# Kernel tuning notes

Measured on AMD Instinct MI355X. Metric: run time of the kernel, lower is better.

The kernel has to match this reference:

```python
import jax, jax.numpy as jnp
import numpy as np

T = 2048          # tokens (prefill, single sequence)
H = 4096          # hidden_size
NH = 32           # num attention heads
NKV = 8           # num kv heads (GQA)
HD = H // NH      # head_dim = 128
EPS = 1e-5
THETA = 10000.0


def setup_inputs() -> dict:
    key = jax.random.key(0)
    k0, k1, k2 = jax.random.split(key, 3)
    return {
        "positions": jnp.arange(T, dtype=jnp.int64 if jax.config.jax_enable_x64 else jnp.int32),
        "hidden_states": jax.random.normal(k0, (T, H), dtype=jnp.float32),
        "w_qkv": jax.random.normal(k1, (H, (NH + 2 * NKV) * HD), dtype=jnp.float32) * 0.02,
        "w_o": jax.random.normal(k2, (NH * HD, H), dtype=jnp.float32) * 0.02,
        "q_norm_w": jnp.ones((NH, HD), dtype=jnp.float32),
        "k_norm_w": jnp.ones((NKV, HD), dtype=jnp.float32),
    }


def _layer_norm(x, w, eps):
    # x: [T, n_heads, HD], w: [n_heads, HD]; mean/var over last dim, fp32 math
    xf = x.astype(jnp.float32)
    mean = xf.mean(-1, keepdims=True)
    var = jnp.square(xf - mean).mean(-1, keepdims=True)
    y = (xf - mean) * jax.lax.rsqrt(var + eps)
    return (w.astype(jnp.float32)[None] * y).astype(x.dtype)


def _rope_interleaved(x, positions):
    # non-neox (GPT-J) style: rotate interleaved pairs. x: [T, n, HD]
    inv_freq = 1.0 / (THETA ** (jnp.arange(0, HD, 2, dtype=jnp.float32) / HD))  # [HD/2]
    freqs = positions.astype(jnp.float32)[:, None] * inv_freq[None, :]          # [T, HD/2]
    cos = jnp.cos(freqs)[:, None, :]  # [T,1,HD/2]
    sin = jnp.sin(freqs)[:, None, :]
    x1 = x[..., 0::2]
    x2 = x[..., 1::2]
    o1 = x1 * cos - x2 * sin
    o2 = x2 * cos + x1 * sin
    return jnp.stack([o1, o2], axis=-1).reshape(x.shape)


def reference(positions, hidden_states, w_qkv, w_o, q_norm_w, k_norm_w):
    qkv = hidden_states @ w_qkv  # [T, (NH+2*NKV)*HD]
    q, k, v = jnp.split(qkv, [NH * HD, (NH + NKV) * HD], axis=-1)
    q = q.reshape(T, NH, HD)
    k = k.reshape(T, NKV, HD)
    v = v.reshape(T, NKV, HD)

    # per-head qk LayerNorm
    q = _layer_norm(q, q_norm_w, EPS)
    k = _layer_norm(k, k_norm_w, EPS)

    # non-neox RoPE
    q = _rope_interleaved(q, positions)
    k = _rope_interleaved(k, positions)

    # GQA: expand kv heads to NH
    rep = NH // NKV
    k = jnp.repeat(k, rep, axis=1)  # [T, NH, HD]
    v = jnp.repeat(v, rep, axis=1)

    scale = HD ** -0.5
    scores = jnp.einsum("qhd,khd->hqk", q * scale, k)  # [NH, T, T]
    causal = jnp.tril(jnp.ones((T, T), dtype=bool))
    scores = jnp.where(causal[None], scores, jnp.finfo(scores.dtype).min)
    probs = jax.nn.softmax(scores, axis=-1)
    attn = jnp.einsum("hqk,khd->qhd", probs, v).reshape(T, NH * HD)

    return attn @ w_o  # [T, H]
```

## Files before the change

### kernel.cpp

```cpp
#include <hip/hip_runtime.h>
#include <cstdint>
#include <cstddef>

#define T_SEQ   2048
#define H_DIM   4096
#define NH_Q    32
#define NKV_H   8
#define HD_     128
#define QKV_N   6144
#define EPS_F   1e-5f
#define ATT_SCALE 0.08838834764831845f
#define LN_THETA  9.210340371976184f

typedef __attribute__((ext_vector_type(8))) short bf16x8;
typedef __attribute__((ext_vector_type(4))) float f32x4;

static __device__ __forceinline__ unsigned short f2bf(float f) {
  union { float f; uint32_t u; } v; v.f = f;
  uint32_t u = v.u;
  u += 0x7fff + ((u >> 16) & 1);
  return (unsigned short)(u >> 16);
}
static __device__ __forceinline__ float bf2f(unsigned short h) {
  union { uint32_t u; float f; } v; v.u = ((uint32_t)h) << 16;
  return v.f;
}

static __device__ __forceinline__ void gld_lds16(const void* g, void* l) {
  __builtin_amdgcn_global_load_lds(
      (const __attribute__((address_space(1))) unsigned int*)g,
      (__attribute__((address_space(3))) unsigned int*)l, 16, 0, 0);
}

__global__ void convert_bf16_kernel(const float* __restrict__ in,
                                    unsigned short* __restrict__ out, int n4) {
  int i = blockIdx.x * blockDim.x + threadIdx.x;
  if (i < n4) {
    float4 f = *(const float4*)(in + (size_t)i * 4);
    ushort4 o;
    o.x = f2bf(f.x); o.y = f2bf(f.y); o.z = f2bf(f.z); o.w = f2bf(f.w);
    *(ushort4*)(out + (size_t)i * 4) = o;
  }
}

__global__ void transpose_bf16_kernel(const float* __restrict__ in,
                                      unsigned short* __restrict__ out,
                                      int R, int C) {
  __shared__ float tile[32][33];
  int c0 = blockIdx.x * 32, r0 = blockIdx.y * 32;
  int tx = threadIdx.x, ty = threadIdx.y;
  for (int i = 0; i < 32; i += 8)
    tile[ty + i][tx] = in[(size_t)(r0 + ty + i) * C + c0 + tx];
  __syncthreads();
  for (int i = 0; i < 32; i += 8)
    out[(size_t)(c0 + ty + i) * R + r0 + tx] = f2bf(tile[tx][ty + i]);
}

template <int FC, int PHASES, bool BF16OUT>
__global__ __launch_bounds__(512) void gemm256_kernel(
    const unsigned short* __restrict__ A, const unsigned short* __restrict__ Bt,
    void* __restrict__ Cp, int M, int N, int K) {
  constexpr int BN = FC * 64;
  constexpr int FR_PER = 8 / PHASES;
  __shared__ unsigned short As[2][256 * 64];
  __shared__ unsigned short Bs[2][BN * 64];
  const int tid = threadIdx.x, lane = tid & 63, wid = tid >> 6;
  const int wm = wid >> 2, wn = wid & 3;
  const int g = lane >> 4, s = lane & 15, s7 = s & 7;
  const int m0 = blockIdx.y * 256, n0 = blockIdx.x * BN;
  const int NT = K >> 6;

  const int lr = lane >> 3, lc = lane & 7;
  const size_t srcoff = (size_t)lr * K + (size_t)((lc ^ lr) * 8);

  auto stage_A_half = [&](const unsigned short* gbase, unsigned short* dst,
                          int h) {
    const int r0 = wid * 32 + h * 16;
    gld_lds16(gbase + (size_t)r0 * K + srcoff, dst + r0 * 64);
    gld_lds16(gbase + (size_t)(r0 + 8) * K + srcoff, dst + (r0 + 8) * 64);
  };
  auto stage_B = [&](const unsigned short* gbase, unsigned short* dst) {
#pragma unroll
    for (int j = 0; j < FC; j++) {
      const int r0 = wid * (FC * 8) + j * 8;
      gld_lds16(gbase + (size_t)r0 * K + srcoff, dst + r0 * 64);
    }
  };

  const int aroff = (wm * 128 + s) * 64;
  const int broff = (wn * FC * 16 + s) * 64;
  const int ck0 = ((0 * 4 + g) ^ s7) * 8;
  const int ck1 = ((1 * 4 + g) ^ s7) * 8;

  f32x4 acc[8][FC] = {};

  stage_A_half(A + (size_t)m0 * K, &As[0][0], 0);
  stage_A_half(A + (size_t)m0 * K, &As[0][0], 1);
  stage_B(Bt + (size_t)n0 * K, &Bs[0][0]);
  stage_B(Bt + (size_t)n0 * K + 64, &Bs[1][0]);
  if constexpr (FC == 2) asm volatile("s_waitcnt vmcnt(2)" ::: "memory");
  else                   asm volatile("s_waitcnt vmcnt(3)" ::: "memory");
  __builtin_amdgcn_s_barrier();

  auto tile_step = [&](int t, unsigned short* cA, unsigned short* cB,
                       unsigned short* nA) {
    const int k0 = t << 6;
    bf16x8 bfr[FC][2];
#pragma unroll
    for (int p = 0; p < PHASES; p++) {
      if (p == 0) {
#pragma unroll
        for (int fc = 0; fc < FC; fc++) {
          bfr[fc][0] = *(const bf16x8*)(cB + broff + fc * 1024 + ck0);
          bfr[fc][1] = *(const bf16x8*)(cB + broff + fc * 1024 + ck1);
        }
      }
      bf16x8 a[FR_PER][2];
#pragma unroll
      for (int i = 0; i < FR_PER; i++) {
        const int fr = p * FR_PER + i;
        a[i][0] = *(const bf16x8*)(cA + aroff + fr * 1024 + ck0);
        a[i][1] = *(const bf16x8*)(cA + aroff + fr * 1024 + ck1);
      }
      if (t + 1 < NT) {
        if (PHASES == 2) {
          if (p == 0) {
            stage_A_half(A + (size_t)m0 * K + k0 + 64, nA, 0);
            stage_A_half(A + (size_t)m0 * K + k0 + 64, nA, 1);
          }
        } else {
          if (p == 0) stage_A_half(A + (size_t)m0 * K + k0 + 64, nA, 0);
          if (p == 1) stage_A_half(A + (size_t)m0 * K + k0 + 64, nA, 1);
        }
      }
      if (p == PHASES - 1 && t + 2 < NT)
        stage_B(Bt + (size_t)n0 * K + k0 + 128, cB);
      __builtin_amdgcn_s_barrier();
      __builtin_amdgcn_s_setprio(1);
#pragma unroll
      for (int i = 0; i < FR_PER; i++) {
        const int fr = p * FR_PER + i;
#pragma unroll
        for (int fc = 0; fc < FC; fc++)
          acc[fr][fc] = __builtin_amdgcn_mfma_f32_16x16x32_bf16(
              a[i][0], bfr[fc][0], acc[fr][fc], 0, 0, 0);
      }
#pragma unroll
      for (int i = 0; i < FR_PER; i++) {
        const int fr = p * FR_PER + i;
#pragma unroll
        for (int fc = 0; fc < FC; fc++)
          acc[fr][fc] = __builtin_amdgcn_mfma_f32_16x16x32_bf16(
              a[i][1], bfr[fc][1], acc[fr][fc], 0, 0, 0);
      }
      __builtin_amdgcn_s_setprio(0);
      if (p == PHASES - 1) {
        if (t + 2 < NT) {
          if constexpr (FC == 2) asm volatile("s_waitcnt vmcnt(2)" ::: "memory");
          else                   asm volatile("s_waitcnt vmcnt(3)" ::: "memory");
        } else {
          asm volatile("s_waitcnt vmcnt(0)" ::: "memory");
        }
      }
      __builtin_amdgcn_s_barrier();
    }
  };

  for (int t = 0; t < NT; t += 2) {
    tile_step(t,     &As[0][0], &Bs[0][0], &As[1][0]);
    tile_step(t + 1, &As[1][0], &Bs[1][0], &As[0][0]);
  }

#pragma unroll
  for (int fr = 0; fr < 8; fr++)
#pragma unroll
    for (int fc = 0; fc < FC; fc++)
#pragma unroll
      for (int r = 0; r < 4; r++) {
        int m = m0 + wm * 128 + fr * 16 + g * 4 + r;
        int n = n0 + wn * FC * 16 + fc * 16 + s;
        float v = acc[fr][fc][r];
        if (BF16OUT) ((unsigned short*)Cp)[(size_t)m * N + n] = f2bf(v);
        else         ((float*)Cp)[(size_t)m * N + n] = v;
      }
}

__global__ __launch_bounds__(256) void ln_rope_kernel(
    unsigned short* __restrict__ qkv, const int* __restrict__ positions,
    const float* __restrict__ qw, const float* __restrict__ kw) {
  const int wid = threadIdx.x >> 6, lane = threadIdx.x & 63;
  const int rid = blockIdx.x * 4 + wid;
  const int t = rid / 40, hh = rid % 40;
  const bool isq = hh < NH_Q;
  const int col = isq ? hh * HD_ : H_DIM + (hh - NH_Q) * HD_;
  unsigned short* row = qkv + (size_t)t * QKV_N + col;

  uint32_t both = *(const uint32_t*)(row + lane * 2);
  float x1 = bf2f((unsigned short)(both & 0xffff));
  float x2 = bf2f((unsigned short)(both >> 16));
  float ssum = x1 + x2, ssq = x1 * x1 + x2 * x2;
  for (int off = 1; off < 64; off <<= 1) {
    ssum += __shfl_xor(ssum, off, 64);
    ssq  += __shfl_xor(ssq,  off, 64);
  }
  float mean = ssum * (1.0f / HD_);
  float var  = ssq * (1.0f / HD_) - mean * mean;
  float rs = rsqrtf(var + EPS_F);
  const float* w = isq ? (qw + hh * HD_) : (kw + (hh - NH_Q) * HD_);
  float2 wv = *(const float2*)(w + lane * 2);
  float y1 = (x1 - mean) * rs * wv.x;
  float y2 = (x2 - mean) * rs * wv.y;
  float pos = (float)positions[t];
  float inv = __expf(-((float)(2 * lane) * (1.0f / HD_)) * LN_THETA);
  float fr = pos * inv;
  float c = cosf(fr), sn = sinf(fr);
  float o1 = y1 * c - y2 * sn;
  float o2 = y2 * c + y1 * sn;
  if (isq) { o1 *= ATT_SCALE; o2 *= ATT_SCALE; }
  *(uint32_t*)(row + lane * 2) =
      (uint32_t)f2bf(o1) | ((uint32_t)f2bf(o2) << 16);
}

__global__ void vt_kernel(const unsigned short* __restrict__ qkv,
                          unsigned short* __restrict__ vt) {
  __shared__ unsigned short tile[32][33];
  const int kvh = blockIdx.z;
  const int t0 = blockIdx.x * 32, d0 = blockIdx.y * 32;
  const int tx = threadIdx.x, ty = threadIdx.y;
  for (int i = 0; i < 32; i += 8)
    tile[ty + i][tx] =
        qkv[(size_t)(t0 + ty + i) * QKV_N + H_DIM + NKV_H * HD_ + kvh * HD_ + d0 + tx];
  __syncthreads();
  for (int i = 0; i < 32; i += 8)
    vt[((size_t)kvh * HD_ + d0 + ty + i) * T_SEQ + t0 + tx] = tile[tx][ty + i];
}

__global__ __launch_bounds__(256) void attn_kernel(
    const unsigned short* __restrict__ qkv, const unsigned short* __restrict__ vt,
    unsigned short* __restrict__ out) {
  __shared__ unsigned short Ks[64 * 136];
  __shared__ unsigned short Vs[128 * 72];
  __shared__ unsigned short Ps[4][16 * 72];
  const int tid = threadIdx.x, lane = tid & 63, wid = tid >> 6;
  const int g = lane >> 4, s = lane & 15;
  const int h = blockIdx.y;
  const int kvh = h >> 2;
  const int NQT = T_SEQ / 64;

  for (int half = 0; half < 2; half++) {
    const int qt = (half == 0) ? (int)blockIdx.x : NQT - 1 - (int)blockIdx.x;
    const int q0 = qt * 64;

    bf16x8 qf[4];
    {
      const unsigned short* qrow =
          qkv + (size_t)(q0 + wid * 16 + s) * QKV_N + h * HD_;
      for (int ks = 0; ks < 4; ks++)
        qf[ks] = *(const bf16x8*)(qrow + ks * 32 + g * 8);
    }
    f32x4 o[8] = {};
    float m_i[4], l_i[4];
    for (int r = 0; r < 4; r++) { m_i[r] = -1e30f; l_i[r] = 0.f; }

    const int ktiles = qt + 1;
    for (int kt = 0; kt < ktiles; kt++) {
      const int k0 = kt * 64;
      __syncthreads();
      {
        int kr = tid >> 4, kc = tid & 15;
        for (int p = 0; p < 4; p++) {
          bf16x8 v = *(const bf16x8*)(qkv + (size_t)(k0 + kr + p * 16) * QKV_N +
                                      H_DIM + kvh * HD_ + kc * 8);
          *(bf16x8*)&Ks[(kr + p * 16) * 136 + kc * 8] = v;
        }
        int vr = tid >> 3, vc = tid & 7;
        for (int p = 0; p < 4; p++) {
          bf16x8 v = *(const bf16x8*)(vt + ((size_t)kvh * HD_ + vr + p * 32) * T_SEQ +
                                      k0 + vc * 8);
          *(bf16x8*)&Vs[(vr + p * 32) * 72 + vc * 8] = v;
        }
      }
      __syncthreads();
      f32x4 sa[4] = {};
      __builtin_amdgcn_s_setprio(1);
      for (int nt = 0; nt < 4; nt++)
        for (int ks = 0; ks < 4; ks++) {
          bf16x8 kb = *(const bf16x8*)&Ks[(nt * 16 + s) * 136 + ks * 32 + g * 8];
          sa[nt] = __builtin_amdgcn_mfma_f32_16x16x32_bf16(qf[ks], kb, sa[nt], 0, 0, 0);
        }
      __builtin_amdgcn_s_setprio(0);
      if (kt == ktiles - 1) {
        for (int nt = 0; nt < 4; nt++)
          for (int r = 0; r < 4; r++)
            if (k0 + nt * 16 + s > q0 + wid * 16 + g * 4 + r) sa[nt][r] = -1e30f;
      }
      float alpha[4];
      for (int r = 0; r < 4; r++) {
        float mx = fmaxf(fmaxf(sa[0][r], sa[1][r]), fmaxf(sa[2][r], sa[3][r]));
        for (int off = 1; off < 16; off <<= 1) mx = fmaxf(mx, __shfl_xor(mx, off, 64));
        float mn = fmaxf(m_i[r], mx);
        alpha[r] = __expf(m_i[r] - mn);
        m_i[r] = mn;
        float rsum = 0.f;
        for (int nt = 0; nt < 4; nt++) {
          float p = __expf(sa[nt][r] - mn);
          sa[nt][r] = p;
          rsum += p;
        }
        for (int off = 1; off < 16; off <<= 1) rsum += __shfl_xor(rsum, off, 64);
        l_i[r] = l_i[r] * alpha[r] + rsum;
      }
      for (int nt = 0; nt < 4; nt++)
        for (int r = 0; r < 4; r++)
          Ps[wid][(g * 4 + r) * 72 + nt * 16 + s] = f2bf(sa[nt][r]);
      for (int ot = 0; ot < 8; ot++)
        for (int r = 0; r < 4; r++) o[ot][r] *= alpha[r];
      __syncthreads();
      __builtin_amdgcn_s_setprio(1);
      for (int ot = 0; ot < 8; ot++)
        for (int ks = 0; ks < 2; ks++) {
          bf16x8 pa = *(const bf16x8*)&Ps[wid][s * 72 + ks * 32 + g * 8];
          bf16x8 vb = *(const bf16x8*)&Vs[(ot * 16 + s) * 72 + ks * 32 + g * 8];
          o[ot] = __builtin_amdgcn_mfma_f32_16x16x32_bf16(pa, vb, o[ot], 0, 0, 0);
        }
      __builtin_amdgcn_s_setprio(0);
    }
    const size_t obase = (size_t)(q0 + wid * 16);
    for (int ot = 0; ot < 8; ot++)
      for (int r = 0; r < 4; r++) {
        float v = o[ot][r] / l_i[r];
        out[(obase + g * 4 + r) * (size_t)(NH_Q * HD_) + h * HD_ + ot * 16 + s] =
            f2bf(v);
      }
  }
}

extern "C" void kernel_launch(void* const* d_in, const int* in_sizes, int n_in,
                              void* d_out, int out_size, void* d_ws, size_t ws_size,
                              hipStream_t stream) {
  const int*   positions = (const int*)d_in[0];
  const float* hs        = (const float*)d_in[1];
  const float* w_qkv     = (const float*)d_in[2];
  const float* w_o       = (const float*)d_in[3];
  const float* q_norm_w  = (const float*)d_in[4];
  const float* k_norm_w  = (const float*)d_in[5];
  float* out = (float*)d_out;

  char* p = (char*)d_ws;
  unsigned short* hsb   = (unsigned short*)p; p += (size_t)T_SEQ * H_DIM * 2;
  unsigned short* wqkvT = (unsigned short*)p; p += (size_t)QKV_N * H_DIM * 2;
  unsigned short* woT   = (unsigned short*)p; p += (size_t)H_DIM * H_DIM * 2;
  unsigned short* qkvb  = (unsigned short*)p; p += (size_t)T_SEQ * QKV_N * 2;
  unsigned short* attnb = (unsigned short*)p; p += (size_t)T_SEQ * H_DIM * 2;
  unsigned short* vtb   = (unsigned short*)p; p += (size_t)NKV_H * HD_ * T_SEQ * 2;

  convert_bf16_kernel<<<(T_SEQ * H_DIM / 4 + 255) / 256, 256, 0, stream>>>(
      hs, hsb, T_SEQ * H_DIM / 4);
  transpose_bf16_kernel<<<dim3(QKV_N / 32, H_DIM / 32), dim3(32, 8), 0, stream>>>(
      w_qkv, wqkvT, H_DIM, QKV_N);
  transpose_bf16_kernel<<<dim3(H_DIM / 32, H_DIM / 32), dim3(32, 8), 0, stream>>>(
      w_o, woT, H_DIM, H_DIM);
  gemm256_kernel<3, 4, true><<<dim3(QKV_N / 192, T_SEQ / 256), 512, 0, stream>>>(
      hsb, wqkvT, qkvb, T_SEQ, QKV_N, H_DIM);
  ln_rope_kernel<<<T_SEQ * (NH_Q + NKV_H) / 4, 256, 0, stream>>>(
      qkvb, positions, q_norm_w, k_norm_w);
  vt_kernel<<<dim3(T_SEQ / 32, HD_ / 32, NKV_H), dim3(32, 8), 0, stream>>>(qkvb, vtb);
  attn_kernel<<<dim3(T_SEQ / 128, NH_Q), 256, 0, stream>>>(qkvb, vtb, attnb);
  gemm256_kernel<2, 2, false><<<dim3(H_DIM / 128, T_SEQ / 256), 512, 0, stream>>>(
      attnb, woT, out, T_SEQ, H_DIM, H_DIM);
}
```

Before: 566.0 us.

## Triple-buffer A tiles in GEMM to prefetch two K-steps ahead

Replaces the phased GEMM mainloop with a pipeline that uses three LDS buffers for A and two for B. The A tile for step t+2 is issued at the start of each step, and B for t+2 is issued after the first fragment's MFMAs. The aim is to hide more global-load latency behind compute and to drop a barrier per phase. The cost is more LDS per block (an extra 32KB A buffer), which may lower occupancy, and a buffer rotation across six unrolled steps that has to stay correct.

Result: slower. 1.538 ms (+171.7%).

```diff
diff --git a/kernel.cpp b/kernel.cpp
--- a/kernel.cpp
+++ b/kernel.cpp
@@ -56,13 +56,12 @@
     out[(size_t)(c0 + ty + i) * R + r0 + tx] = f2bf(tile[tx][ty + i]);
 }
 
-template <int FC, int PHASES, bool BF16OUT>
-__global__ __launch_bounds__(512) void gemm256_kernel(
+template <int FC, bool BF16OUT>
+__global__ __launch_bounds__(512) void gemm_pipe_kernel(
     const unsigned short* __restrict__ A, const unsigned short* __restrict__ Bt,
     void* __restrict__ Cp, int M, int N, int K) {
   constexpr int BN = FC * 64;
-  constexpr int FR_PER = 8 / PHASES;
-  __shared__ unsigned short As[2][256 * 64];
+  __shared__ unsigned short As[3][256 * 64];
   __shared__ unsigned short Bs[2][BN * 64];
   const int tid = threadIdx.x, lane = tid & 63, wid = tid >> 6;
   const int wm = wid >> 2, wn = wid & 3;
@@ -73,17 +72,18 @@
   const int lr = lane >> 3, lc = lane & 7;
   const size_t srcoff = (size_t)lr * K + (size_t)((lc ^ lr) * 8);
 
-  auto stage_A_half = [&](const unsigned short* gbase, unsigned short* dst,
-                          int h) {
-    const int r0 = wid * 32 + h * 16;
-    gld_lds16(gbase + (size_t)r0 * K + srcoff, dst + r0 * 64);
-    gld_lds16(gbase + (size_t)(r0 + 8) * K + srcoff, dst + (r0 + 8) * 64);
+  auto stage_A = [&](const unsigned short* gk, unsigned short* dst) {
+#pragma unroll
+    for (int j = 0; j < 4; j++) {
+      const int r0 = wid * 32 + j * 8;
+      gld_lds16(gk + (size_t)r0 * K + srcoff, dst + r0 * 64);
+    }
   };
-  auto stage_B = [&](const unsigned short* gbase, unsigned short* dst) {
+  auto stage_B = [&](const unsigned short* gk, unsigned short* dst) {
 #pragma unroll
     for (int j = 0; j < FC; j++) {
       const int r0 = wid * (FC * 8) + j * 8;
-      gld_lds16(gbase + (size_t)r0 * K + srcoff, dst + r0 * 64);
+      gld_lds16(gk + (size_t)r0 * K + srcoff, dst + r0 * 64);
     }
   };
 
@@ -94,81 +94,79 @@
 
   f32x4 acc[8][FC] = {};
 
-  stage_A_half(A + (size_t)m0 * K, &As[0][0], 0);
-  stage_A_half(A + (size_t)m0 * K, &As[0][0], 1);
+  stage_A(A + (size_t)m0 * K, &As[0][0]);
   stage_B(Bt + (size_t)n0 * K, &Bs[0][0]);
+  stage_A(A + (size_t)m0 * K + 64, &As[1][0]);
   stage_B(Bt + (size_t)n0 * K + 64, &Bs[1][0]);
-  if constexpr (FC == 2) asm volatile("s_waitcnt vmcnt(2)" ::: "memory");
-  else                   asm volatile("s_waitcnt vmcnt(3)" ::: "memory");
+  if constexpr (FC == 2) asm volatile("s_waitcnt vmcnt(6)" ::: "memory");
+  else                   asm volatile("s_waitcnt vmcnt(7)" ::: "memory");
   __builtin_amdgcn_s_barrier();
 
   auto tile_step = [&](int t, unsigned short* cA, unsigned short* cB,
                        unsigned short* nA) {
     const int k0 = t << 6;
+    if (t + 2 < NT) stage_A(A + (size_t)m0 * K + k0 + 128, nA);
     bf16x8 bfr[FC][2];
 #pragma unroll
-    for (int p = 0; p < PHASES; p++) {
-      if (p == 0) {
-#pragma unroll
-        for (int fc = 0; fc < FC; fc++) {
-          bfr[fc][0] = *(const bf16x8*)(cB + broff + fc * 1024 + ck0);
-          bfr[fc][1] = *(const bf16x8*)(cB + broff + fc * 1024 + ck1);
-        }
-      }
-      bf16x8 a[FR_PER][2];
-#pragma unroll
-      for (int i = 0; i < FR_PER; i++) {
-        const int fr = p * FR_PER + i;
-        a[i][0] = *(const bf16x8*)(cA + aroff + fr * 1024 + ck0);
-        a[i][1] = *(const bf16x8*)(cA + aroff + fr * 1024 + ck1);
-      }
-      if (t + 1 < NT) {
-        if (PHASES == 2) {
-          if (p == 0) {
-            stage_A_half(A + (size_t)m0 * K + k0 + 64, nA, 0);
-            stage_A_half(A + (size_t)m0 * K + k0 + 64, nA, 1);
-          }
-        } else {
-          if (p == 0) stage_A_half(A + (size_t)m0 * K + k0 + 64, nA, 0);
-          if (p == 1) stage_A_half(A + (size_t)m0 * K + k0 + 64, nA, 1);
-        }
-      }
-      if (p == PHASES - 1 && t + 2 < NT)
-        stage_B(Bt + (size_t)n0 * K + k0 + 128, cB);
-      __builtin_amdgcn_s_barrier();
+    for (int fc = 0; fc < FC; fc++) {
+      bfr[fc][0] = *(const bf16x8*)(cB + broff + fc * 1024 + ck0);
+      bfr[fc][1] = *(const bf16x8*)(cB + broff + fc * 1024 + ck1);
+    }
+    {
+      bf16x8 a00 = *(const bf16x8*)(cA + aroff + 0 * 1024 + ck0);
+      bf16x8 a01 = *(const bf16x8*)(cA + aroff + 0 * 1024 + ck1);
+      bf16x8 a10 = *(const bf16x8*)(cA + aroff + 1 * 1024 + ck0);
+      bf16x8 a11 = *(const bf16x8*)(cA + aroff + 1 * 1024 + ck1);
       __builtin_amdgcn_s_setprio(1);
 #pragma unroll
-      for (int i = 0; i < FR_PER; i++) {
-        const int fr = p * FR_PER + i;
-#pragma unroll
-        for (int fc = 0; fc < FC; fc++)
-          acc[fr][fc] = __builtin_amdgcn_mfma_f32_16x16x32_bf16(
-              a[i][0], bfr[fc][0], acc[fr][fc], 0, 0, 0);
-      }
-#pragma unroll
-      for (int i = 0; i < FR_PER; i++) {
-        const int fr = p * FR_PER + i;
-#pragma unroll
-        for (int fc = 0; fc < FC; fc++)
-          acc[fr][fc] = __builtin_amdgcn_mfma_f32_16x16x32_bf16(
-              a[i][1], bfr[fc][1], acc[fr][fc], 0, 0, 0);
+      for (int fc = 0; fc < FC; fc++) {
+        acc[0][fc] = __builtin_amdgcn_mfma_f32_16x16x32_bf16(a00, bfr[fc][0], acc[0][fc], 0, 0, 0);
+        acc[1][fc] = __builtin_amdgcn_mfma_f32_16x16x32_bf16(a10, bfr[fc][0], acc[1][fc], 0, 0, 0);
+      }
+#pragma unroll
+      for (int fc = 0; fc < FC; fc++) {
+        acc[0][fc] = __builtin_amdgcn_mfma_f32_16x16x32_bf16(a01, bfr[fc][1], acc[0][fc], 0, 0, 0);
+        acc[1][fc] = __builtin_amdgcn_mfma_f32_16x16x32_bf16(a11, bfr[fc][1], acc[1][fc], 0, 0, 0);
       }
       __builtin_amdgcn_s_setprio(0);
-      if (p == PHASES - 1) {
-        if (t + 2 < NT) {
-          if constexpr (FC == 2) asm volatile("s_waitcnt vmcnt(2)" ::: "memory");
-          else                   asm volatile("s_waitcnt vmcnt(3)" ::: "memory");
-        } else {
-          asm volatile("s_waitcnt vmcnt(0)" ::: "memory");
-        }
-      }
-      __builtin_amdgcn_s_barrier();
-    }
+    }
+    __builtin_amdgcn_s_barrier();
+    if (t + 2 < NT) stage_B(Bt + (size_t)n0 * K + k0 + 128, cB);
+#pragma unroll
+    for (int p = 1; p < 4; p++) {
+      bf16x8 a00 = *(const bf16x8*)(cA + aroff + (2 * p) * 1024 + ck0);
+      bf16x8 a01 = *(const bf16x8*)(cA + aroff + (2 * p) * 1024 + ck1);
+      bf16x8 a10 = *(const bf16x8*)(cA + aroff + (2 * p + 1) * 1024 + ck0);
+      bf16x8 a11 = *(const bf16x8*)(cA + aroff + (2 * p + 1) * 1024 + ck1);
+      __builtin_amdgcn_s_setprio(1);
+#pragma unroll
+      for (int fc = 0; fc < FC; fc++) {
+        acc[2 * p][fc]     = __builtin_amdgcn_mfma_f32_16x16x32_bf16(a00, bfr[fc][0], acc[2 * p][fc], 0, 0, 0);
+        acc[2 * p + 1][fc] = __builtin_amdgcn_mfma_f32_16x16x32_bf16(a10, bfr[fc][0], acc[2 * p + 1][fc], 0, 0, 0);
+      }
+#pragma unroll
+      for (int fc = 0; fc < FC; fc++) {
+        acc[2 * p][fc]     = __builtin_amdgcn_mfma_f32_16x16x32_bf16(a01, bfr[fc][1], acc[2 * p][fc], 0, 0, 0);
+        acc[2 * p + 1][fc] = __builtin_amdgcn_mfma_f32_16x16x32_bf16(a11, bfr[fc][1], acc[2 * p + 1][fc], 0, 0, 0);
+      }
+      __builtin_amdgcn_s_setprio(0);
+    }
+    if (t + 2 < NT) {
+      if constexpr (FC == 2) asm volatile("s_waitcnt vmcnt(6)" ::: "memory");
+      else                   asm volatile("s_waitcnt vmcnt(7)" ::: "memory");
+    } else {
+      asm volatile("s_waitcnt vmcnt(0)" ::: "memory");
+    }
+    __builtin_amdgcn_s_barrier();
   };
 
-  for (int t = 0; t < NT; t += 2) {
-    tile_step(t,     &As[0][0], &Bs[0][0], &As[1][0]);
-    tile_step(t + 1, &As[1][0], &Bs[1][0], &As[0][0]);
+  for (int t = 0; t < NT;) {
+    tile_step(t, &As[0][0], &Bs[0][0], &As[2][0]); if (++t == NT) break;
+    tile_step(t, &As[1][0], &Bs[1][0], &As[0][0]); if (++t == NT) break;
+    tile_step(t, &As[2][0], &Bs[0][0], &As[1][0]); if (++t == NT) break;
+    tile_step(t, &As[0][0], &Bs[1][0], &As[2][0]); if (++t == NT) break;
+    tile_step(t, &As[1][0], &Bs[0][0], &As[0][0]); if (++t == NT) break;
+    tile_step(t, &As[2][0], &Bs[1][0], &As[1][0]); if (++t == NT) break;
   }
 
 #pragma unroll
@@ -360,12 +358,12 @@
       w_qkv, wqkvT, H_DIM, QKV_N);
   transpose_bf16_kernel<<<dim3(H_DIM / 32, H_DIM / 32), dim3(32, 8), 0, stream>>>(
       w_o, woT, H_DIM, H_DIM);
-  gemm256_kernel<3, 4, true><<<dim3(QKV_N / 192, T_SEQ / 256), 512, 0, stream>>>(
+  gemm_pipe_kernel<3, true><<<dim3(QKV_N / 192, T_SEQ / 256), 512, 0, stream>>>(
       hsb, wqkvT, qkvb, T_SEQ, QKV_N, H_DIM);
   ln_rope_kernel<<<T_SEQ * (NH_Q + NKV_H) / 4, 256, 0, stream>>>(
       qkvb, positions, q_norm_w, k_norm_w);
   vt_kernel<<<dim3(T_SEQ / 32, HD_ / 32, NKV_H), dim3(32, 8), 0, stream>>>(qkvb, vtb);
   attn_kernel<<<dim3(T_SEQ / 128, NH_Q), 256, 0, stream>>>(qkvb, vtb, attnb);
-  gemm256_kernel<2, 2, false><<<dim3(H_DIM / 128, T_SEQ / 256), 512, 0, stream>>>(
+  gemm_pipe_kernel<2, false><<<dim3(H_DIM / 128, T_SEQ / 256), 512, 0, stream>>>(
       attnb, woT, out, T_SEQ, H_DIM, H_DIM);
 }
```
